# Performance work log

Measured on AMD Instinct MI355X. Metric: run time of the kernel, lower is better.

The kernel has to match this reference:

```python
import jax, jax.numpy as jnp
import numpy as np

B, LQ, LKV, D, DV = 8, 2048, 2048, 128, 128


def setup_inputs() -> dict:
    key = jax.random.key(0)
    kq, kk, kv = jax.random.split(key, 3)
    return {
        "query": jax.random.normal(kq, (B, LQ, D), dtype=jnp.float32),
        "key": jax.random.normal(kk, (B, LKV, D), dtype=jnp.float32),
        "value": jax.random.normal(kv, (B, LKV, DV), dtype=jnp.float32),
    }


def reference(query, key, value):
    # score_fn: scaled dot-product  score = Q K^T / sqrt(Dq)
    scale = 1.0 / jnp.sqrt(jnp.asarray(query.shape[-1], query.dtype))
    score = jnp.einsum("bqd,bkd->bqk", query, key) * scale  # (B, Lq, Lkv)
    attention_weights = jax.nn.softmax(score, axis=-1)
    context_vector = jnp.einsum("bqk,bkv->bqv", attention_weights, value)
    return attention_weights, context_vector
```

## Files before the change

### kernel.cpp

```cpp
#include <hip/hip_runtime.h>

#define BB    8
#define LQN   2048
#define LKVN  2048
#define DQ    128
#define DVN   128
#define QT    16
#define KVW   32
#define KTI   128
#define NT    (LKVN / KTI)
#define KSTR  136
#define OSTR  132

typedef short short8 __attribute__((ext_vector_type(8)));
typedef float f32x4  __attribute__((ext_vector_type(4)));
typedef int   int4v  __attribute__((ext_vector_type(4)));

__device__ __forceinline__ short f2bf(float f) {
  unsigned u = __builtin_bit_cast(unsigned, f);
  u += 0x7fffu + ((u >> 16) & 1u);
  return (short)(u >> 16);
}

__device__ __forceinline__ int packbf(float a, float b) {
  unsigned lo = (unsigned short)f2bf(a);
  unsigned hi = (unsigned short)f2bf(b);
  return (int)(lo | (hi << 16));
}

__global__ __launch_bounds__(256) void pre_kernel(const float* __restrict__ K,
                                                  const float* __restrict__ V,
                                                  short* __restrict__ Kb,
                                                  short* __restrict__ Vt) {
  __shared__ float tile[128][33];
  if (blockIdx.x >= 512) {
    int i = (blockIdx.x - 512) * 256 + threadIdx.x;
    size_t off = (size_t)i * 8;
    float4 a = *(const float4*)(K + off);
    float4 c = *(const float4*)(K + off + 4);
    short8 o;
    o[0] = f2bf(a.x); o[1] = f2bf(a.y); o[2] = f2bf(a.z); o[3] = f2bf(a.w);
    o[4] = f2bf(c.x); o[5] = f2bf(c.y); o[6] = f2bf(c.z); o[7] = f2bf(c.w);
    *(short8*)(Kb + off) = o;
    return;
  }
  const int bx  = blockIdx.x;
  const int kv0 = (bx & 15) * 128;
  const int dv0 = ((bx >> 4) & 3) * 32;
  const int b   = bx >> 6;
  const int tid = threadIdx.x;
  const float* src = V + ((size_t)b * LKVN + kv0) * DVN + dv0;
#pragma unroll
  for (int it = 0; it < 4; ++it) {
    int idx = it * 256 + tid;
    int r = idx >> 3, c4 = idx & 7;
    float4 v = *(const float4*)(src + (size_t)r * DVN + c4 * 4);
    tile[r][c4 * 4 + 0] = v.x;
    tile[r][c4 * 4 + 1] = v.y;
    tile[r][c4 * 4 + 2] = v.z;
    tile[r][c4 * 4 + 3] = v.w;
  }
  __syncthreads();
  short* dst = Vt + ((size_t)b * DVN + dv0) * LKVN + kv0;
#pragma unroll
  for (int it = 0; it < 2; ++it) {
    int idx = it * 256 + tid;
    int row = idx >> 4, ch = idx & 15;
    short8 o;
#pragma unroll
    for (int j = 0; j < 8; ++j) o[j] = f2bf(tile[ch * 8 + j][row]);
    *(short8*)(dst + (size_t)row * LKVN + ch * 8) = o;
  }
}

__global__ __launch_bounds__(256, 3) void attn_kernel(const float* __restrict__ Q,
                                                      const short* __restrict__ Kb,
                                                      const short* __restrict__ Vt,
                                                      float* __restrict__ W,
                                                      float* __restrict__ O) {
  __shared__ __align__(16) char smem[KTI * KSTR * 2];
  __shared__ float red_l[4][QT];
  short (*k_lds)[KSTR] = (short (*)[KSTR])smem;
  float (*osum)[QT][OSTR] = (float (*)[QT][OSTR])smem;

  const int tid  = threadIdx.x;
  const int w    = tid >> 6;
  const int lane = tid & 63;
  const int n    = lane & 15;
  const int qd   = lane >> 4;
  const int b    = blockIdx.x & 7;
  const int q0   = (blockIdx.x >> 3) * QT;

  const short* Kbase = Kb + (size_t)b * LKVN * DQ;
  const short* Vw = Vt + ((size_t)b * DVN + n) * LKVN + w * KVW + qd * 8;
  float* Wrow = W + ((size_t)b * LQN + q0 + n) * LKVN + w * KVW + qd * 4;

  const int sr = tid >> 4;
  const int sc = (tid & 15) * 8;

  short8 qf[4];
  {
    const float* Qrow = Q + ((size_t)b * LQN + q0 + n) * DQ + qd * 8;
#pragma unroll
    for (int ks = 0; ks < 4; ++ks) {
      float4 f0 = *(const float4*)(Qrow + ks * 32);
      float4 f1 = *(const float4*)(Qrow + ks * 32 + 4);
      short8 o;
      o[0] = f2bf(f0.x); o[1] = f2bf(f0.y); o[2] = f2bf(f0.z); o[3] = f2bf(f0.w);
      o[4] = f2bf(f1.x); o[5] = f2bf(f1.y); o[6] = f2bf(f1.z); o[7] = f2bf(f1.w);
      qf[ks] = o;
    }
  }

  const float scale = 0.08838834764831845f;
  float l_part = 0.f;
  short8 kreg[8];

#pragma unroll
  for (int j = 0; j < 8; ++j)
    kreg[j] = *(const short8*)(Kbase + (size_t)(j * 16 + sr) * DQ + sc);
#pragma unroll
  for (int j = 0; j < 8; ++j)
    *(short8*)&k_lds[j * 16 + sr][sc] = kreg[j];

  for (int t = 0; t < NT; ++t) {
    __syncthreads();
    if (t + 1 < NT) {
      const short* src = Kbase + (size_t)(t + 1) * KTI * DQ;
#pragma unroll
      for (int j = 0; j < 8; ++j)
        kreg[j] = *(const short8*)(src + (size_t)(j * 16 + sr) * DQ + sc);
    }
#pragma unroll
    for (int t2 = 0; t2 < 2; ++t2) {
      f32x4 acc = {0.f, 0.f, 0.f, 0.f};
#pragma unroll
      for (int ks = 0; ks < 4; ++ks) {
        short8 kf = *(const short8*)&k_lds[w * KVW + t2 * 16 + n][ks * 32 + qd * 8];
        acc = __builtin_amdgcn_mfma_f32_16x16x32_bf16(kf, qf[ks], acc, 0, 0, 0);
      }
#pragma unroll
      for (int r = 0; r < 4; ++r) l_part += __expf(acc[r] * scale);
    }
    __syncthreads();
    if (t + 1 < NT) {
#pragma unroll
      for (int j = 0; j < 8; ++j)
        *(short8*)&k_lds[j * 16 + sr][sc] = kreg[j];
    }
  }

  l_part += __shfl_xor(l_part, 16, 64);
  l_part += __shfl_xor(l_part, 32, 64);
  if (lane < 16) red_l[w][lane] = l_part;
  __syncthreads();
  const float rinv = 1.0f / (red_l[0][n] + red_l[1][n] + red_l[2][n] + red_l[3][n]);

  const int srcA = n + ((qd & 1) << 5);
  const int srcB = srcA + 16;
  const int sel  = qd >> 1;

  f32x4 oacc[8];
#pragma unroll
  for (int dvg = 0; dvg < 8; ++dvg) oacc[dvg] = (f32x4){0.f, 0.f, 0.f, 0.f};

#pragma unroll
  for (int j = 0; j < 8; ++j)
    kreg[j] = *(const short8*)(Kbase + (size_t)(j * 16 + sr) * DQ + sc);
#pragma unroll
  for (int j = 0; j < 8; ++j)
    *(short8*)&k_lds[j * 16 + sr][sc] = kreg[j];

  for (int t = 0; t < NT; ++t) {
    __syncthreads();
    f32x4 acc[2];
    __builtin_amdgcn_s_setprio(1);
#pragma unroll
    for (int t2 = 0; t2 < 2; ++t2) {
      acc[t2] = (f32x4){0.f, 0.f, 0.f, 0.f};
#pragma unroll
      for (int ks = 0; ks < 4; ++ks) {
        short8 kf = *(const short8*)&k_lds[w * KVW + t2 * 16 + n][ks * 32 + qd * 8];
        acc[t2] = __builtin_amdgcn_mfma_f32_16x16x32_bf16(kf, qf[ks], acc[t2], 0, 0, 0);
      }
    }
    __builtin_amdgcn_s_setprio(0);

    if (t + 1 < NT) {
      const short* src = Kbase + (size_t)(t + 1) * KTI * DQ;
#pragma unroll
      for (int j = 0; j < 8; ++j)
        kreg[j] = *(const short8*)(src + (size_t)(j * 16 + sr) * DQ + sc);
    }
    short8 vf[8];
#pragma unroll
    for (int dvg = 0; dvg < 8; ++dvg)
      vf[dvg] = *(const short8*)(Vw + (size_t)(dvg * 16) * LKVN + t * KTI);

    int pk[2][2];
#pragma unroll
    for (int t2 = 0; t2 < 2; ++t2) {
      float p0 = __expf(acc[t2][0] * scale) * rinv;
      float p1 = __expf(acc[t2][1] * scale) * rinv;
      float p2 = __expf(acc[t2][2] * scale) * rinv;
      float p3 = __expf(acc[t2][3] * scale) * rinv;
      f32x4 st = {p0, p1, p2, p3};
      *(f32x4*)(Wrow + t * KTI + t2 * 16) = st;
      pk[t2][0] = packbf(p0, p1);
      pk[t2][1] = packbf(p2, p3);
    }
    int a0 = __shfl(pk[0][0], srcA, 64);
    int b0 = __shfl(pk[1][0], srcA, 64);
    int a1 = __shfl(pk[0][1], srcA, 64);
    int b1 = __shfl(pk[1][1], srcA, 64);
    int a2 = __shfl(pk[0][0], srcB, 64);
    int b2 = __shfl(pk[1][0], srcB, 64);
    int a3 = __shfl(pk[0][1], srcB, 64);
    int b3 = __shfl(pk[1][1], srcB, 64);
    int4v bi;
    bi[0] = sel ? b0 : a0;
    bi[1] = sel ? b1 : a1;
    bi[2] = sel ? b2 : a2;
    bi[3] = sel ? b3 : a3;
    short8 bfr = __builtin_bit_cast(short8, bi);

    __builtin_amdgcn_s_setprio(1);
#pragma unroll
    for (int dvg = 0; dvg < 8; ++dvg)
      oacc[dvg] = __builtin_amdgcn_mfma_f32_16x16x32_bf16(vf[dvg], bfr, oacc[dvg], 0, 0, 0);
    __builtin_amdgcn_s_setprio(0);

    __syncthreads();
    if (t + 1 < NT) {
#pragma unroll
      for (int j = 0; j < 8; ++j)
        *(short8*)&k_lds[j * 16 + sr][sc] = kreg[j];
    }
  }

  if (w < 2) {
#pragma unroll
    for (int dvg = 0; dvg < 8; ++dvg)
      *(f32x4*)&osum[w][n][dvg * 16 + qd * 4] = oacc[dvg];
  }
  __syncthreads();
  if (w >= 2) {
#pragma unroll
    for (int dvg = 0; dvg < 8; ++dvg) {
      f32x4* p = (f32x4*)&osum[w - 2][n][dvg * 16 + qd * 4];
      *p = *p + oacc[dvg];
    }
  }
  __syncthreads();

  float* Ob = O + ((size_t)b * LQN + q0) * DVN;
  const int qq = tid >> 4;
  const int c0 = (tid & 15) * 8;
#pragma unroll
  for (int c = 0; c < 2; ++c) {
    f32x4 s0 = *(const f32x4*)&osum[0][qq][c0 + c * 4];
    f32x4 s1 = *(const f32x4*)&osum[1][qq][c0 + c * 4];
    s0 = s0 + s1;
    *(f32x4*)(Ob + (size_t)qq * DVN + c0 + c * 4) = s0;
  }
}

extern "C" void kernel_launch(void* const* d_in, const int* in_sizes, int n_in,
                              void* d_out, int out_size, void* d_ws, size_t ws_size,
                              hipStream_t stream) {
  const float* Q = (const float*)d_in[0];
  const float* K = (const float*)d_in[1];
  const float* V = (const float*)d_in[2];
  float* W = (float*)d_out;
  float* O = W + (size_t)BB * LQN * LKVN;
  short* Kb = (short*)d_ws;
  short* Vt = Kb + (size_t)BB * LKVN * DQ;

  pre_kernel<<<1536, 256, 0, stream>>>(K, V, Kb, Vt);
  attn_kernel<<<1024, 256, 0, stream>>>(Q, Kb, Vt, W, O);
}
```

Before: 251.9 us.

## Double query tile per block to share K tiles and swizzle K in LDS

Raises the query tile from 16 to 32 rows by running 512 threads as two groups of four warps over the same K tile in LDS. Each staged K tile now serves twice as many queries, which cuts global K loads and LDS fills per query. The padded K layout is replaced with an XOR swizzle to avoid bank conflicts without extra LDS. In exchange the grid is half as many larger blocks, which changes occupancy and adds more threads waiting at each barrier.

```diff
diff --git a/kernel.cpp b/kernel.cpp
--- a/kernel.cpp
+++ b/kernel.cpp
@@ -5,11 +5,9 @@
 #define LKVN  2048
 #define DQ    128
 #define DVN   128
-#define QT    16
-#define KVW   32
+#define QT    32
 #define KTI   128
 #define NT    (LKVN / KTI)
-#define KSTR  136
 #define OSTR  132
 
 typedef short short8 __attribute__((ext_vector_type(8)));
@@ -73,14 +71,14 @@
   }
 }
 
-__global__ __launch_bounds__(256, 3) void attn_kernel(const float* __restrict__ Q,
+__global__ __launch_bounds__(512, 4) void attn_kernel(const float* __restrict__ Q,
                                                       const short* __restrict__ Kb,
                                                       const short* __restrict__ Vt,
                                                       float* __restrict__ W,
                                                       float* __restrict__ O) {
-  __shared__ __align__(16) char smem[KTI * KSTR * 2];
+  __shared__ __align__(16) char smem[33792];
   __shared__ float red_l[4][QT];
-  short (*k_lds)[KSTR] = (short (*)[KSTR])smem;
+  short* k_lds = (short*)smem;
   float (*osum)[QT][OSTR] = (float (*)[QT][OSTR])smem;
 
   const int tid  = threadIdx.x;
@@ -88,19 +86,25 @@
   const int lane = tid & 63;
   const int n    = lane & 15;
   const int qd   = lane >> 4;
+  const int s    = w & 3;
+  const int g    = w >> 2;
   const int b    = blockIdx.x & 7;
   const int q0   = (blockIdx.x >> 3) * QT;
 
   const short* Kbase = Kb + (size_t)b * LKVN * DQ;
-  const short* Vw = Vt + ((size_t)b * DVN + n) * LKVN + w * KVW + qd * 8;
-  float* Wrow = W + ((size_t)b * LQN + q0 + n) * LKVN + w * KVW + qd * 4;
+  const short* Vw = Vt + ((size_t)b * DVN + n) * LKVN + s * 32 + qd * 8;
+  float* Wrow = W + ((size_t)b * LQN + q0 + g * 16 + n) * LKVN + s * 32 + qd * 4;
 
   const int sr = tid >> 4;
-  const int sc = (tid & 15) * 8;
+  const int sc = tid & 15;
+  const int swz_w = (sc * 8) ^ ((sr & 7) << 3);
+
+  const int krow = s * 32 + n;
+  const int rswz = (n & 7) << 3;
 
   short8 qf[4];
   {
-    const float* Qrow = Q + ((size_t)b * LQN + q0 + n) * DQ + qd * 8;
+    const float* Qrow = Q + ((size_t)b * LQN + q0 + g * 16 + n) * DQ + qd * 8;
 #pragma unroll
     for (int ks = 0; ks < 4; ++ks) {
       float4 f0 = *(const float4*)(Qrow + ks * 32);
@@ -114,29 +118,30 @@
 
   const float scale = 0.08838834764831845f;
   float l_part = 0.f;
-  short8 kreg[8];
-
-#pragma unroll
-  for (int j = 0; j < 8; ++j)
-    kreg[j] = *(const short8*)(Kbase + (size_t)(j * 16 + sr) * DQ + sc);
-#pragma unroll
-  for (int j = 0; j < 8; ++j)
-    *(short8*)&k_lds[j * 16 + sr][sc] = kreg[j];
+  short8 kreg[4];
+
+#pragma unroll
+  for (int j = 0; j < 4; ++j)
+    kreg[j] = *(const short8*)(Kbase + (size_t)(j * 32 + sr) * DQ + sc * 8);
+#pragma unroll
+  for (int j = 0; j < 4; ++j)
+    *(short8*)&k_lds[(j * 32 + sr) * 128 + swz_w] = kreg[j];
 
   for (int t = 0; t < NT; ++t) {
     __syncthreads();
     if (t + 1 < NT) {
       const short* src = Kbase + (size_t)(t + 1) * KTI * DQ;
 #pragma unroll
-      for (int j = 0; j < 8; ++j)
-        kreg[j] = *(const short8*)(src + (size_t)(j * 16 + sr) * DQ + sc);
+      for (int j = 0; j < 4; ++j)
+        kreg[j] = *(const short8*)(src + (size_t)(j * 32 + sr) * DQ + sc * 8);
     }
 #pragma unroll
     for (int t2 = 0; t2 < 2; ++t2) {
       f32x4 acc = {0.f, 0.f, 0.f, 0.f};
 #pragma unroll
       for (int ks = 0; ks < 4; ++ks) {
-        short8 kf = *(const short8*)&k_lds[w * KVW + t2 * 16 + n][ks * 32 + qd * 8];
+        short8 kf = *(const short8*)&k_lds[(krow + t2 * 16) * 128 +
+                                           ((ks * 32 + qd * 8) ^ rswz)];
         acc = __builtin_amdgcn_mfma_f32_16x16x32_bf16(kf, qf[ks], acc, 0, 0, 0);
       }
 #pragma unroll
@@ -145,16 +150,18 @@
     __syncthreads();
     if (t + 1 < NT) {
 #pragma unroll
-      for (int j = 0; j < 8; ++j)
-        *(short8*)&k_lds[j * 16 + sr][sc] = kreg[j];
+      for (int j = 0; j < 4; ++j)
+        *(short8*)&k_lds[(j * 32 + sr) * 128 + swz_w] = kreg[j];
     }
   }
 
   l_part += __shfl_xor(l_part, 16, 64);
   l_part += __shfl_xor(l_part, 32, 64);
-  if (lane < 16) red_l[w][lane] = l_part;
-  __syncthreads();
-  const float rinv = 1.0f / (red_l[0][n] + red_l[1][n] + red_l[2][n] + red_l[3][n]);
+  if (lane < 16) red_l[s][g * 16 + lane] = l_part;
+  __syncthreads();
+  const float rinv =
+      1.0f / (red_l[0][g * 16 + n] + red_l[1][g * 16 + n] +
+              red_l[2][g * 16 + n] + red_l[3][g * 16 + n]);
 
   const int srcA = n + ((qd & 1) << 5);
   const int srcB = srcA + 16;
@@ -165,11 +172,11 @@
   for (int dvg = 0; dvg < 8; ++dvg) oacc[dvg] = (f32x4){0.f, 0.f, 0.f, 0.f};
 
 #pragma unroll
-  for (int j = 0; j < 8; ++j)
-    kreg[j] = *(const short8*)(Kbase + (size_t)(j * 16 + sr) * DQ + sc);
-#pragma unroll
-  for (int j = 0; j < 8; ++j)
-    *(short8*)&k_lds[j * 16 + sr][sc] = kreg[j];
+  for (int j = 0; j < 4; ++j)
+    kreg[j] = *(const short8*)(Kbase + (size_t)(j * 32 + sr) * DQ + sc * 8);
+#pragma unroll
+  for (int j = 0; j < 4; ++j)
+    *(short8*)&k_lds[(j * 32 + sr) * 128 + swz_w] = kreg[j];
 
   for (int t = 0; t < NT; ++t) {
     __syncthreads();
@@ -180,7 +187,8 @@
       acc[t2] = (f32x4){0.f, 0.f, 0.f, 0.f};
 #pragma unroll
       for (int ks = 0; ks < 4; ++ks) {
-        short8 kf = *(const short8*)&k_lds[w * KVW + t2 * 16 + n][ks * 32 + qd * 8];
+        short8 kf = *(const short8*)&k_lds[(krow + t2 * 16) * 128 +
+                                           ((ks * 32 + qd * 8) ^ rswz)];
         acc[t2] = __builtin_amdgcn_mfma_f32_16x16x32_bf16(kf, qf[ks], acc[t2], 0, 0, 0);
       }
     }
@@ -189,8 +197,8 @@
     if (t + 1 < NT) {
       const short* src = Kbase + (size_t)(t + 1) * KTI * DQ;
 #pragma unroll
-      for (int j = 0; j < 8; ++j)
-        kreg[j] = *(const short8*)(src + (size_t)(j * 16 + sr) * DQ + sc);
+      for (int j = 0; j < 4; ++j)
+        kreg[j] = *(const short8*)(src + (size_t)(j * 32 + sr) * DQ + sc * 8);
     }
     short8 vf[8];
 #pragma unroll
@@ -233,21 +241,21 @@
     __syncthreads();
     if (t + 1 < NT) {
 #pragma unroll
-      for (int j = 0; j < 8; ++j)
-        *(short8*)&k_lds[j * 16 + sr][sc] = kreg[j];
-    }
-  }
-
-  if (w < 2) {
+      for (int j = 0; j < 4; ++j)
+        *(short8*)&k_lds[(j * 32 + sr) * 128 + swz_w] = kreg[j];
+    }
+  }
+
+  if (s < 2) {
 #pragma unroll
     for (int dvg = 0; dvg < 8; ++dvg)
-      *(f32x4*)&osum[w][n][dvg * 16 + qd * 4] = oacc[dvg];
-  }
-  __syncthreads();
-  if (w >= 2) {
+      *(f32x4*)&osum[s][g * 16 + n][dvg * 16 + qd * 4] = oacc[dvg];
+  }
+  __syncthreads();
+  if (s >= 2) {
 #pragma unroll
     for (int dvg = 0; dvg < 8; ++dvg) {
-      f32x4* p = (f32x4*)&osum[w - 2][n][dvg * 16 + qd * 4];
+      f32x4* p = (f32x4*)&osum[s - 2][g * 16 + n][dvg * 16 + qd * 4];
       *p = *p + oacc[dvg];
     }
   }
@@ -277,5 +285,5 @@
   short* Vt = Kb + (size_t)BB * LKVN * DQ;
 
   pre_kernel<<<1536, 256, 0, stream>>>(K, V, Kb, Vt);
-  attn_kernel<<<1024, 256, 0, stream>>>(Q, Kb, Vt, W, O);
-}
+  attn_kernel<<<512, 512, 0, stream>>>(Q, Kb, Vt, W, O);
+}
```

Measured after the change: 236.5 us. -6.1%, faster.

## Swizzle K tile in LDS and overlap second-pass K prefetch with reduction

Applied to the files above, without the earlier changes.

Replaces the padded K tile in shared memory (stride 136) with an unpadded 128-wide layout. The column chunk is XOR-swizzled by row to avoid bank conflicts, and the swizzle is applied on the global read side. The first K tile of the second pass is now loaded before the row-sum reduction barrier, and V loads are issued before the next K prefetch. Occupancy is now set with waves_per_eu(4,4) instead of min 3 blocks, which may constrain registers differently.

```diff
diff --git a/kernel.cpp b/kernel.cpp
--- a/kernel.cpp
+++ b/kernel.cpp
@@ -6,10 +6,8 @@
 #define DQ    128
 #define DVN   128
 #define QT    16
-#define KVW   32
 #define KTI   128
 #define NT    (LKVN / KTI)
-#define KSTR  136
 #define OSTR  132
 
 typedef short short8 __attribute__((ext_vector_type(8)));
@@ -73,15 +71,16 @@
   }
 }
 
-__global__ __launch_bounds__(256, 3) void attn_kernel(const float* __restrict__ Q,
-                                                      const short* __restrict__ Kb,
-                                                      const short* __restrict__ Vt,
-                                                      float* __restrict__ W,
-                                                      float* __restrict__ O) {
-  __shared__ __align__(16) char smem[KTI * KSTR * 2];
+__global__ __launch_bounds__(256)
+__attribute__((amdgpu_waves_per_eu(4, 4)))
+void attn_kernel(const float* __restrict__ Q,
+                 const short* __restrict__ Kb,
+                 const short* __restrict__ Vt,
+                 float* __restrict__ W,
+                 float* __restrict__ O) {
+  __shared__ __align__(16) short k_lds[KTI * 128];
   __shared__ float red_l[4][QT];
-  short (*k_lds)[KSTR] = (short (*)[KSTR])smem;
-  float (*osum)[QT][OSTR] = (float (*)[QT][OSTR])smem;
+  float (*osum)[QT][OSTR] = (float (*)[QT][OSTR])k_lds;
 
   const int tid  = threadIdx.x;
   const int w    = tid >> 6;
@@ -92,11 +91,15 @@
   const int q0   = (blockIdx.x >> 3) * QT;
 
   const short* Kbase = Kb + (size_t)b * LKVN * DQ;
-  const short* Vw = Vt + ((size_t)b * DVN + n) * LKVN + w * KVW + qd * 8;
-  float* Wrow = W + ((size_t)b * LQN + q0 + n) * LKVN + w * KVW + qd * 4;
-
-  const int sr = tid >> 4;
-  const int sc = (tid & 15) * 8;
+  const short* Vw = Vt + ((size_t)b * DVN + n) * LKVN + w * 32 + qd * 8;
+  float* Wrow = W + ((size_t)b * LQN + q0 + n) * LKVN + w * 32 + qd * 4;
+
+  const int srow  = tid >> 4;
+  const int scol8 = (tid & 15) * 8;
+  const int gsrc8 = ((tid & 15) ^ (srow & 7)) * 8;
+
+  const int krow = (w * 32 + n) * 128;
+  const int rswz = (n & 7) << 3;
 
   short8 qf[4];
   {
@@ -116,45 +119,42 @@
   float l_part = 0.f;
   short8 kreg[8];
 
-#pragma unroll
-  for (int j = 0; j < 8; ++j)
-    kreg[j] = *(const short8*)(Kbase + (size_t)(j * 16 + sr) * DQ + sc);
-#pragma unroll
-  for (int j = 0; j < 8; ++j)
-    *(short8*)&k_lds[j * 16 + sr][sc] = kreg[j];
-
+#define KLOAD(t)                                                                \
+  _Pragma("unroll")                                                             \
+  for (int j = 0; j < 8; ++j)                                                   \
+    kreg[j] = *(const short8*)(Kbase + (size_t)((t) * KTI + j * 16 + srow) * DQ + gsrc8);
+#define KWRITE()                                                                \
+  _Pragma("unroll")                                                             \
+  for (int j = 0; j < 8; ++j)                                                   \
+    *(short8*)&k_lds[(j * 16 + srow) * 128 + scol8] = kreg[j];
+
+  KLOAD(0)
+  KWRITE()
   for (int t = 0; t < NT; ++t) {
     __syncthreads();
-    if (t + 1 < NT) {
-      const short* src = Kbase + (size_t)(t + 1) * KTI * DQ;
-#pragma unroll
-      for (int j = 0; j < 8; ++j)
-        kreg[j] = *(const short8*)(src + (size_t)(j * 16 + sr) * DQ + sc);
-    }
+    if (t + 1 < NT) KLOAD(t + 1)
 #pragma unroll
     for (int t2 = 0; t2 < 2; ++t2) {
       f32x4 acc = {0.f, 0.f, 0.f, 0.f};
 #pragma unroll
       for (int ks = 0; ks < 4; ++ks) {
-        short8 kf = *(const short8*)&k_lds[w * KVW + t2 * 16 + n][ks * 32 + qd * 8];
+        short8 kf = *(const short8*)&k_lds[krow + t2 * 2048 + ((ks * 32 + qd * 8) ^ rswz)];
         acc = __builtin_amdgcn_mfma_f32_16x16x32_bf16(kf, qf[ks], acc, 0, 0, 0);
       }
 #pragma unroll
       for (int r = 0; r < 4; ++r) l_part += __expf(acc[r] * scale);
     }
     __syncthreads();
-    if (t + 1 < NT) {
-#pragma unroll
-      for (int j = 0; j < 8; ++j)
-        *(short8*)&k_lds[j * 16 + sr][sc] = kreg[j];
-    }
+    if (t + 1 < NT) KWRITE()
   }
 
   l_part += __shfl_xor(l_part, 16, 64);
   l_part += __shfl_xor(l_part, 32, 64);
   if (lane < 16) red_l[w][lane] = l_part;
+  KLOAD(0)
   __syncthreads();
   const float rinv = 1.0f / (red_l[0][n] + red_l[1][n] + red_l[2][n] + red_l[3][n]);
+  KWRITE()
 
   const int srcA = n + ((qd & 1) << 5);
   const int srcB = srcA + 16;
@@ -164,13 +164,6 @@
 #pragma unroll
   for (int dvg = 0; dvg < 8; ++dvg) oacc[dvg] = (f32x4){0.f, 0.f, 0.f, 0.f};
 
-#pragma unroll
-  for (int j = 0; j < 8; ++j)
-    kreg[j] = *(const short8*)(Kbase + (size_t)(j * 16 + sr) * DQ + sc);
-#pragma unroll
-  for (int j = 0; j < 8; ++j)
-    *(short8*)&k_lds[j * 16 + sr][sc] = kreg[j];
-
   for (int t = 0; t < NT; ++t) {
     __syncthreads();
     f32x4 acc[2];
@@ -180,22 +173,17 @@
       acc[t2] = (f32x4){0.f, 0.f, 0.f, 0.f};
 #pragma unroll
       for (int ks = 0; ks < 4; ++ks) {
-        short8 kf = *(const short8*)&k_lds[w * KVW + t2 * 16 + n][ks * 32 + qd * 8];
+        short8 kf = *(const short8*)&k_lds[krow + t2 * 2048 + ((ks * 32 + qd * 8) ^ rswz)];
         acc[t2] = __builtin_amdgcn_mfma_f32_16x16x32_bf16(kf, qf[ks], acc[t2], 0, 0, 0);
       }
     }
     __builtin_amdgcn_s_setprio(0);
 
-    if (t + 1 < NT) {
-      const short* src = Kbase + (size_t)(t + 1) * KTI * DQ;
-#pragma unroll
-      for (int j = 0; j < 8; ++j)
-        kreg[j] = *(const short8*)(src + (size_t)(j * 16 + sr) * DQ + sc);
-    }
     short8 vf[8];
 #pragma unroll
     for (int dvg = 0; dvg < 8; ++dvg)
       vf[dvg] = *(const short8*)(Vw + (size_t)(dvg * 16) * LKVN + t * KTI);
+    if (t + 1 < NT) KLOAD(t + 1)
 
     int pk[2][2];
 #pragma unroll
@@ -231,11 +219,7 @@
     __builtin_amdgcn_s_setprio(0);
 
     __syncthreads();
-    if (t + 1 < NT) {
-#pragma unroll
-      for (int j = 0; j < 8; ++j)
-        *(short8*)&k_lds[j * 16 + sr][sc] = kreg[j];
-    }
+    if (t + 1 < NT) KWRITE()
   }
 
   if (w < 2) {
```

Result: slower. 298.0 us (+18.3%).
